# Kernel tuning notes

Measured on AMD Instinct MI355X. Metric: run time of the kernel, lower is better.

## Reference

```python
import math
import jax, jax.numpy as jnp
import numpy as np

ANCHOR_AREAS = [4 * 4, 16 * 16, 64 * 64, 128 * 128]
ASPECT_RATIOS = [1 / 2.0, 1 / 1.0, 2 / 1.0]
SCALE_RATIOS = [1.0, 2.0, 3 / 4.0]
NUM_ANCHORS = len(ASPECT_RATIOS) * len(SCALE_RATIOS)  # 9


def _anchor_wh():
    wh = []
    for s in ANCHOR_AREAS:
        for ar in ASPECT_RATIOS:
            h = math.sqrt(s / ar)
            w = ar * h
            for sr in SCALE_RATIOS:
                wh.append([w * sr, h * sr])
    return np.asarray(wh, np.float32).reshape(len(ANCHOR_AREAS), NUM_ANCHORS, 2)


def build_anchor_boxes(input_size):
    """All anchors in (cx, cy, w, h), shape [A, 4]. Static numpy computation."""
    wh = _anchor_wh()
    out = []
    for i in range(len(ANCHOR_AREAS)):
        fm = int(math.ceil(input_size / 2.0 ** (i + 2)))
        grid = input_size / fm
        centers = (np.arange(fm, dtype=np.float32) + 0.5) * grid
        gx, gy = np.meshgrid(centers, centers)  # gx varies along width
        xy = np.stack([gx, gy], axis=-1)  # [fm, fm, 2]
        xy = np.broadcast_to(xy[:, :, None, :], (fm, fm, NUM_ANCHORS, 2))
        whl = np.broadcast_to(wh[i][None, None, :, :], (fm, fm, NUM_ANCHORS, 2))
        out.append(np.concatenate([xy, whl], axis=-1).reshape(-1, 4))
    return jnp.asarray(np.concatenate(out, 0), jnp.float32)


def box_iou_xywh(anchors, boxes):
    """anchors [A,4] xywh, boxes [B,N,4] xywh -> IoU [B,A,N] (kuangliu +1 convention)."""
    a1 = jnp.concatenate([anchors[:, :2] - anchors[:, 2:] / 2,
                          anchors[:, :2] + anchors[:, 2:] / 2], axis=-1)  # [A,4]
    b1 = jnp.concatenate([boxes[..., :2] - boxes[..., 2:] / 2,
                          boxes[..., :2] + boxes[..., 2:] / 2], axis=-1)  # [B,N,4]
    lt = jnp.maximum(a1[None, :, None, :2], b1[:, None, :, :2])  # [B,A,N,2]
    rb = jnp.minimum(a1[None, :, None, 2:], b1[:, None, :, 2:])
    wh = jnp.clip(rb - lt + 1.0, 0.0)
    inter = wh[..., 0] * wh[..., 1]  # [B,A,N]
    area_a = (a1[:, 2] - a1[:, 0] + 1.0) * (a1[:, 3] - a1[:, 1] + 1.0)  # [A]
    area_b = (b1[..., 2] - b1[..., 0] + 1.0) * (b1[..., 3] - b1[..., 1] + 1.0)  # [B,N]
    return inter / (area_a[None, :, None] + area_b[:, None, :] - inter)


def setup_inputs() -> dict:
    key = jax.random.key(0)
    k1, k2, k3 = jax.random.split(key, 3)
    B, N, S = 4, 64, 512
    # valid xyxy boxes inside the image
    x1y1 = jax.random.uniform(k1, (B, N, 2), jnp.float32, 0.0, S - 130.0)
    wh = jax.random.uniform(k2, (B, N, 2), jnp.float32, 4.0, 128.0)
    boxes = jnp.concatenate([x1y1, x1y1 + wh], axis=-1)
    labels = jax.random.randint(k3, (B, N), 0, 10, jnp.int64 if jax.config.jax_enable_x64 else jnp.int32)
    return {"labels": labels, "boxes": boxes, "input_size": S}


def reference(labels, boxes, input_size):
    B = boxes.shape[0]
    anchors = build_anchor_boxes(int(input_size))  # [A,4] xywh
    # xyxy -> xywh (kuangliu: center (a+b)/2, size b-a+1)
    a, b = boxes[..., :2], boxes[..., 2:]
    boxes_xywh = jnp.concatenate([(a + b) / 2.0, b - a + 1.0], axis=-1)  # [B,N,4]
    ious = box_iou_xywh(anchors, boxes_xywh)  # [B,A,N]
    max_ious = jnp.max(ious, axis=2)  # [B,A]
    max_ids = jnp.argmax(ious, axis=2)  # [B,A]
    gather = jax.vmap(lambda t, i: t[i])
    matched = gather(boxes_xywh, max_ids)  # [B,A,4]
    loc_xy = (matched[..., :2] - anchors[None, :, :2]) / anchors[None, :, 2:]
    loc_wh = jnp.log(matched[..., 2:] / anchors[None, :, 2:])
    loc_targets = jnp.concatenate([loc_xy, loc_wh], axis=-1)  # [B,A,4]
    cls = gather(labels, max_ids)  # [B,A]
    cls = jnp.where(max_ious < 0.5, 0, cls)
    cls = jnp.where((max_ious > 0.4) & (max_ious < 0.5), -1, cls)
    return cls, loc_targets
```

## Files before the change

### kernel.cpp

```cpp
#include <hip/hip_runtime.h>
#include <math.h>


__global__ __launch_bounds__(256) void anchors_kernel(
    const int*   __restrict__ labels,
    const float* __restrict__ boxes,
    float*       __restrict__ out,
    int B, int N, int A, int S)
{
    __shared__ float4 s_corn[256];
    __shared__ float  s_area[256];
    __shared__ float4 s_xywh[256];
    __shared__ int    s_lab[256];
    __shared__ float4 s_b0[4];
    __shared__ int    s_l0[4];

    const int t    = threadIdx.x;
    const int lane = t & 63;
    const int wid  = t >> 6;
    const int gid  = blockIdx.x * 256 + t;

    const int b  = (blockIdx.x * 256) / A;
    int r0 = blockIdx.x * 256 - b * A;
    int lvl = 0, fm = S >> 2;
    #pragma unroll
    for (int i = 0; i < 3; ++i) {
        int cnt = fm * fm * 9;
        if (r0 >= cnt) { r0 -= cnt; lvl = i + 1; fm >>= 1; }
    }
    const int   lfm  = 31 - __clz(fm);
    const float grid = (float)(4 << lvl);
    const float sl   = (float)((lvl == 3) ? 128 : (4 << (2 * lvl)));

    const int wr0     = r0 + wid * 64;
    const int cell_lo = wr0 / 9;
    const int cell_hi = (wr0 + 63) / 9;
    const int ci_lo = cell_lo >> lfm, ci_hi = cell_hi >> lfm;
    int cj_lo, cj_hi;
    if (ci_lo == ci_hi) { cj_lo = cell_lo & (fm - 1); cj_hi = cell_hi & (fm - 1); }
    else                { cj_lo = 0;                  cj_hi = fm - 1; }
    const float ext  = 1.41422f * sl + 0.5f;
    const float bbx1 = ((float)cj_lo + 0.5f) * grid - ext;
    const float bbx2 = ((float)cj_hi + 0.5f) * grid + ext;
    const float bby1 = ((float)ci_lo + 0.5f) * grid - ext;
    const float bby2 = ((float)ci_hi + 0.5f) * grid + ext;

    int L;
    {
        bool  pred = false;
        float cx = 0, cy = 0, w = 0, h = 0, bx1 = 0, by1 = 0, bx2 = 0, by2 = 0;
        int   lab = 0;
        if (lane < N) {
            float4 bx = reinterpret_cast<const float4*>(boxes)[b * N + lane];
            cx = (bx.x + bx.z) * 0.5f;
            cy = (bx.y + bx.w) * 0.5f;
            w  = bx.z - bx.x + 1.0f;
            h  = bx.w - bx.y + 1.0f;
            bx1 = cx - w * 0.5f;  by1 = cy - h * 0.5f;
            bx2 = cx + w * 0.5f;  by2 = cy + h * 0.5f;
            lab = labels[b * N + lane];
            pred = (fminf(bbx2, bx2) - fmaxf(bbx1, bx1) + 1.0f > 0.0f) &&
                   (fminf(bby2, by2) - fmaxf(bby1, by1) + 1.0f > 0.0f);
        }
        unsigned long long mask = __ballot(pred);
        if (pred) {
            int pos = wid * 64 + __popcll(mask & ((1ull << lane) - 1ull));
            s_corn[pos] = make_float4(bx1, by1, bx2, by2);
            s_area[pos] = (bx2 - bx1 + 1.0f) * (by2 - by1 + 1.0f);
            s_xywh[pos] = make_float4(cx, cy, w, h);
            s_lab[pos]  = lab;
        }
        if (lane == 0) { s_b0[wid] = make_float4(cx, cy, w, h); s_l0[wid] = lab; }
        L = __popcll(mask);
    }

    const int r    = r0 + t;
    const int k    = r % 9;
    const int cell = r / 9;
    const int cj   = cell & (fm - 1);
    const int ci   = cell >> lfm;

    const int ar_i = (k >= 6) ? 2 : ((k >= 3) ? 1 : 0);
    const int sr_i = k - 3 * ar_i;
    const double s2  = sqrt(2.0);
    const double hb  = (ar_i == 0) ? s2 : (ar_i == 1 ? 1.0 : 0.5 * s2);
    const double wb  = (ar_i == 0) ? 0.5 * s2 : (ar_i == 1 ? 1.0 : s2);
    const double srd = (sr_i == 0) ? 1.0 : (sr_i == 1 ? 2.0 : 0.75);
    const float  aw  = (float)(wb * srd) * sl;
    const float  ah  = (float)(hb * srd) * sl;

    const float acx = ((float)cj + 0.5f) * grid;
    const float acy = ((float)ci + 0.5f) * grid;
    const float ax1 = acx - aw * 0.5f;
    const float ay1 = acy - ah * 0.5f;
    const float ax2 = acx + aw * 0.5f;
    const float ay2 = acy + ah * 0.5f;
    const float area_a = (ax2 - ax1 + 1.0f) * (ay2 - ay1 + 1.0f);

    float best_in = 0.0f, best_un = 1.0f;
    int   bj = -1;
    const int base = wid * 64;
    for (int j = 0; j < L; ++j) {
        float4 c = s_corn[base + j];
        float iw = fmaxf(fminf(ax2, c.z) - fmaxf(ax1, c.x) + 1.0f, 0.0f);
        float ih = fmaxf(fminf(ay2, c.w) - fmaxf(ay1, c.y) + 1.0f, 0.0f);
        float in_ = iw * ih;
        float un_ = (area_a + s_area[base + j]) - in_;
        bool better = (in_ * best_un) > (best_in * un_);
        best_in = better ? in_ : best_in;
        best_un = better ? un_ : best_un;
        bj      = better ? j   : bj;
    }

    float best, mcx, mcy, mw, mh;
    int lab;
    if (bj >= 0) {
        best = best_in / best_un;
        float4 m = s_xywh[base + bj];
        mcx = m.x; mcy = m.y; mw = m.z; mh = m.w;
        lab = s_lab[base + bj];
    } else {
        best = 0.0f;
        float4 m = s_b0[wid];
        mcx = m.x; mcy = m.y; mw = m.z; mh = m.w;
        lab = s_l0[wid];
    }

    int cls = lab;
    if (best < 0.5f) cls = 0;
    if (best > 0.4f && best < 0.5f) cls = -1;

    const float rcp_aw = __builtin_amdgcn_rcpf(aw);
    const float rcp_ah = __builtin_amdgcn_rcpf(ah);
    float4 loc;
    loc.x = (mcx - acx) * rcp_aw;
    loc.y = (mcy - acy) * rcp_ah;
    loc.z = __logf(mw * rcp_aw);
    loc.w = __logf(mh * rcp_ah);

    if (gid < B * A) {
        out[(size_t)gid] = (float)cls;
        reinterpret_cast<float4*>(out + (size_t)B * A)[gid] = loc;
    }
}

extern "C" void kernel_launch(void* const* d_in, const int* in_sizes, int n_in,
                              void* d_out, int out_size, void* d_ws, size_t ws_size,
                              hipStream_t stream) {
    const int S = 512;
    int A = 0;
    for (int i = 0; i < 4; ++i) {
        int f = (S + (1 << (i + 2)) - 1) >> (i + 2);
        A += f * f * 9;
    }
    const int B = out_size / (5 * A);
    const int N = in_sizes[0] / B;

    const int total  = B * A;
    const int blocks = (total + 255) / 256;

    anchors_kernel<<<blocks, 256, 0, stream>>>(
        (const int*)d_in[0], (const float*)d_in[1], (float*)d_out, B, N, A, S);
}
```

Before: 17.34 us.

## Coarsen threads to four anchors each with per-wave 256-anchor chunks and 2D grid

Each wave now handles a contiguous chunk of 256 anchors, four per lane, and the batch index comes from blockIdx.y instead of a division. The box load, culling ballot and shared-memory compaction are done once per 256 anchors rather than once per 64, and the inner IoU loop reuses each loaded candidate box across four anchors for more instruction-level parallelism. In exchange, the culling bounding box covers a wider span of anchors, so each wave may keep more candidate boxes, and about a quarter as many threads are launched.

```diff
diff --git a/kernel.cpp b/kernel.cpp
--- a/kernel.cpp
+++ b/kernel.cpp
@@ -18,10 +18,12 @@
     const int t    = threadIdx.x;
     const int lane = t & 63;
     const int wid  = t >> 6;
-    const int gid  = blockIdx.x * 256 + t;
+    const int b    = blockIdx.y;
 
-    const int b  = (blockIdx.x * 256) / A;
-    int r0 = blockIdx.x * 256 - b * A;
+    const int wr0 = (blockIdx.x * 4 + wid) * 256;
+    if (wr0 >= A) return;
+
+    int r0 = wr0;
     int lvl = 0, fm = S >> 2;
     #pragma unroll
     for (int i = 0; i < 3; ++i) {
@@ -32,9 +34,8 @@
     const float grid = (float)(4 << lvl);
     const float sl   = (float)((lvl == 3) ? 128 : (4 << (2 * lvl)));
 
-    const int wr0     = r0 + wid * 64;
-    const int cell_lo = wr0 / 9;
-    const int cell_hi = (wr0 + 63) / 9;
+    const int cell_lo = r0 / 9;
+    const int cell_hi = (r0 + 255) / 9;
     const int ci_lo = cell_lo >> lfm, ci_hi = cell_hi >> lfm;
     int cj_lo, cj_hi;
     if (ci_lo == ci_hi) { cj_lo = cell_lo & (fm - 1); cj_hi = cell_hi & (fm - 1); }
@@ -74,73 +75,81 @@
         L = __popcll(mask);
     }
 
-    const int r    = r0 + t;
-    const int k    = r % 9;
-    const int cell = r / 9;
-    const int cj   = cell & (fm - 1);
-    const int ci   = cell >> lfm;
+    float ax1[4], ay1[4], ax2[4], ay2[4], areaA[4];
+    float awv[4], ahv[4], acxv[4], acyv[4];
+    #pragma unroll
+    for (int q = 0; q < 4; ++q) {
+        const int r    = r0 + 64 * q + lane;
+        const int cell = r / 9;
+        const int kk   = r - cell * 9;
+        const int cj   = cell & (fm - 1);
+        const int ci   = cell >> lfm;
+        const int ar_i = (kk >= 6) ? 2 : ((kk >= 3) ? 1 : 0);
+        const int sr_i = kk - 3 * ar_i;
+        const double s2  = 1.4142135623730951;
+        const double hb  = (ar_i == 0) ? s2 : (ar_i == 1 ? 1.0 : 0.5 * s2);
+        const double wb  = (ar_i == 0) ? 0.5 * s2 : (ar_i == 1 ? 1.0 : s2);
+        const double srd = (sr_i == 0) ? 1.0 : (sr_i == 1 ? 2.0 : 0.75);
+        const float aw  = (float)(wb * srd) * sl;
+        const float ah  = (float)(hb * srd) * sl;
+        const float acx = ((float)cj + 0.5f) * grid;
+        const float acy = ((float)ci + 0.5f) * grid;
+        awv[q] = aw; ahv[q] = ah; acxv[q] = acx; acyv[q] = acy;
+        ax1[q] = acx - aw * 0.5f;  ay1[q] = acy - ah * 0.5f;
+        ax2[q] = acx + aw * 0.5f;  ay2[q] = acy + ah * 0.5f;
+        areaA[q] = (ax2[q] - ax1[q] + 1.0f) * (ay2[q] - ay1[q] + 1.0f);
+    }
 
-    const int ar_i = (k >= 6) ? 2 : ((k >= 3) ? 1 : 0);
-    const int sr_i = k - 3 * ar_i;
-    const double s2  = sqrt(2.0);
-    const double hb  = (ar_i == 0) ? s2 : (ar_i == 1 ? 1.0 : 0.5 * s2);
-    const double wb  = (ar_i == 0) ? 0.5 * s2 : (ar_i == 1 ? 1.0 : s2);
-    const double srd = (sr_i == 0) ? 1.0 : (sr_i == 1 ? 2.0 : 0.75);
-    const float  aw  = (float)(wb * srd) * sl;
-    const float  ah  = (float)(hb * srd) * sl;
-
-    const float acx = ((float)cj + 0.5f) * grid;
-    const float acy = ((float)ci + 0.5f) * grid;
-    const float ax1 = acx - aw * 0.5f;
-    const float ay1 = acy - ah * 0.5f;
-    const float ax2 = acx + aw * 0.5f;
-    const float ay2 = acy + ah * 0.5f;
-    const float area_a = (ax2 - ax1 + 1.0f) * (ay2 - ay1 + 1.0f);
-
-    float best_in = 0.0f, best_un = 1.0f;
-    int   bj = -1;
+    float bin[4] = {0.0f, 0.0f, 0.0f, 0.0f};
+    float bun[4] = {1.0f, 1.0f, 1.0f, 1.0f};
+    int   bj[4]  = {-1, -1, -1, -1};
     const int base = wid * 64;
     for (int j = 0; j < L; ++j) {
-        float4 c = s_corn[base + j];
-        float iw = fmaxf(fminf(ax2, c.z) - fmaxf(ax1, c.x) + 1.0f, 0.0f);
-        float ih = fmaxf(fminf(ay2, c.w) - fmaxf(ay1, c.y) + 1.0f, 0.0f);
-        float in_ = iw * ih;
-        float un_ = (area_a + s_area[base + j]) - in_;
-        bool better = (in_ * best_un) > (best_in * un_);
-        best_in = better ? in_ : best_in;
-        best_un = better ? un_ : best_un;
-        bj      = better ? j   : bj;
+        float4 c  = s_corn[base + j];
+        float  ab = s_area[base + j];
+        #pragma unroll
+        for (int q = 0; q < 4; ++q) {
+            float iw = fmaxf(fminf(ax2[q], c.z) - fmaxf(ax1[q], c.x) + 1.0f, 0.0f);
+            float ih = fmaxf(fminf(ay2[q], c.w) - fmaxf(ay1[q], c.y) + 1.0f, 0.0f);
+            float in_ = iw * ih;
+            float un_ = (areaA[q] + ab) - in_;
+            bool better = (in_ * bun[q]) > (bin[q] * un_);
+            bin[q] = better ? in_ : bin[q];
+            bun[q] = better ? un_ : bun[q];
+            bj[q]  = better ? j   : bj[q];
+        }
     }
 
-    float best, mcx, mcy, mw, mh;
-    int lab;
-    if (bj >= 0) {
-        best = best_in / best_un;
-        float4 m = s_xywh[base + bj];
-        mcx = m.x; mcy = m.y; mw = m.z; mh = m.w;
-        lab = s_lab[base + bj];
-    } else {
-        best = 0.0f;
-        float4 m = s_b0[wid];
-        mcx = m.x; mcy = m.y; mw = m.z; mh = m.w;
-        lab = s_l0[wid];
-    }
+    #pragma unroll
+    for (int q = 0; q < 4; ++q) {
+        float best, mcx, mcy, mw, mh;
+        int lab;
+        if (bj[q] >= 0) {
+            best = bin[q] / bun[q];
+            float4 m = s_xywh[base + bj[q]];
+            mcx = m.x; mcy = m.y; mw = m.z; mh = m.w;
+            lab = s_lab[base + bj[q]];
+        } else {
+            best = 0.0f;
+            float4 m = s_b0[wid];
+            mcx = m.x; mcy = m.y; mw = m.z; mh = m.w;
+            lab = s_l0[wid];
+        }
+        int cls = lab;
+        if (best < 0.5f) cls = 0;
+        if (best > 0.4f && best < 0.5f) cls = -1;
 
-    int cls = lab;
-    if (best < 0.5f) cls = 0;
-    if (best > 0.4f && best < 0.5f) cls = -1;
+        const float rcp_aw = __builtin_amdgcn_rcpf(awv[q]);
+        const float rcp_ah = __builtin_amdgcn_rcpf(ahv[q]);
+        float4 loc;
+        loc.x = (mcx - acxv[q]) * rcp_aw;
+        loc.y = (mcy - acyv[q]) * rcp_ah;
+        loc.z = __logf(mw * rcp_aw);
+        loc.w = __logf(mh * rcp_ah);
 
-    const float rcp_aw = __builtin_amdgcn_rcpf(aw);
-    const float rcp_ah = __builtin_amdgcn_rcpf(ah);
-    float4 loc;
-    loc.x = (mcx - acx) * rcp_aw;
-    loc.y = (mcy - acy) * rcp_ah;
-    loc.z = __logf(mw * rcp_aw);
-    loc.w = __logf(mh * rcp_ah);
-
-    if (gid < B * A) {
-        out[(size_t)gid] = (float)cls;
-        reinterpret_cast<float4*>(out + (size_t)B * A)[gid] = loc;
+        const size_t gidq = (size_t)b * A + (size_t)(wr0 + 64 * q + lane);
+        out[gidq] = (float)cls;
+        reinterpret_cast<float4*>(out + (size_t)B * A)[gidq] = loc;
     }
 }
 
@@ -156,9 +165,10 @@
     const int B = out_size / (5 * A);
     const int N = in_sizes[0] / B;
 
-    const int total  = B * A;
-    const int blocks = (total + 255) / 256;
+    const int chunks  = A / 256;
+    const int blocksX = (chunks + 3) / 4;
+    dim3 gridDim(blocksX, B);
 
-    anchors_kernel<<<blocks, 256, 0, stream>>>(
+    anchors_kernel<<<gridDim, 256, 0, stream>>>(
         (const int*)d_in[0], (const float*)d_in[1], (float*)d_out, B, N, A, S);
 }
```

After: 22.60 us. +30.3%, slower.

## Use 2D grid with 1024-thread blocks and constant anchor-size tables

Applied to the files above, without the earlier changes.

Switches the launch to a 2D grid (anchor chunks by batch) with 1024-thread blocks, so each wave derives its own level and batch and exits early past A. The double-precision sqrt/multiply used for anchor sizes is replaced with float constant selects. The per-wave box culling test now runs on the raw xyxy box before the xywh conversion, with a wider margin. Larger blocks reduce the block count but may lower occupancy flexibility.

```diff
diff --git a/kernel.cpp b/kernel.cpp
--- a/kernel.cpp
+++ b/kernel.cpp
@@ -2,26 +2,28 @@
 #include <math.h>
 
 
-__global__ __launch_bounds__(256) void anchors_kernel(
+__global__ __launch_bounds__(1024) void anchors_kernel(
     const int*   __restrict__ labels,
     const float* __restrict__ boxes,
     float*       __restrict__ out,
     int B, int N, int A, int S)
 {
-    __shared__ float4 s_corn[256];
-    __shared__ float  s_area[256];
-    __shared__ float4 s_xywh[256];
-    __shared__ int    s_lab[256];
-    __shared__ float4 s_b0[4];
-    __shared__ int    s_l0[4];
+    __shared__ float4 s_corn[1024];
+    __shared__ float  s_area[1024];
+    __shared__ float4 s_xywh[1024];
+    __shared__ int    s_lab[1024];
+    __shared__ float4 s_b0[16];
+    __shared__ int    s_l0[16];
 
     const int t    = threadIdx.x;
     const int lane = t & 63;
     const int wid  = t >> 6;
-    const int gid  = blockIdx.x * 256 + t;
+    const int b    = blockIdx.y;
 
-    const int b  = (blockIdx.x * 256) / A;
-    int r0 = blockIdx.x * 256 - b * A;
+    const int wr0 = blockIdx.x * 1024 + wid * 64;
+    if (wr0 >= A) return;
+
+    int r0 = wr0;
     int lvl = 0, fm = S >> 2;
     #pragma unroll
     for (int i = 0; i < 3; ++i) {
@@ -32,14 +34,13 @@
     const float grid = (float)(4 << lvl);
     const float sl   = (float)((lvl == 3) ? 128 : (4 << (2 * lvl)));
 
-    const int wr0     = r0 + wid * 64;
-    const int cell_lo = wr0 / 9;
-    const int cell_hi = (wr0 + 63) / 9;
+    const int cell_lo = r0 / 9;
+    const int cell_hi = (r0 + 63) / 9;
     const int ci_lo = cell_lo >> lfm, ci_hi = cell_hi >> lfm;
     int cj_lo, cj_hi;
     if (ci_lo == ci_hi) { cj_lo = cell_lo & (fm - 1); cj_hi = cell_hi & (fm - 1); }
     else                { cj_lo = 0;                  cj_hi = fm - 1; }
-    const float ext  = 1.41422f * sl + 0.5f;
+    const float ext  = 1.41422f * sl + 2.0f;
     const float bbx1 = ((float)cj_lo + 0.5f) * grid - ext;
     const float bbx2 = ((float)cj_hi + 0.5f) * grid + ext;
     const float bby1 = ((float)ci_lo + 0.5f) * grid - ext;
@@ -52,6 +53,8 @@
         int   lab = 0;
         if (lane < N) {
             float4 bx = reinterpret_cast<const float4*>(boxes)[b * N + lane];
+            pred = (fminf(bbx2, bx.z) - fmaxf(bbx1, bx.x) + 1.0f > 0.0f) &&
+                   (fminf(bby2, bx.w) - fmaxf(bby1, bx.y) + 1.0f > 0.0f);
             cx = (bx.x + bx.z) * 0.5f;
             cy = (bx.y + bx.w) * 0.5f;
             w  = bx.z - bx.x + 1.0f;
@@ -59,8 +62,6 @@
             bx1 = cx - w * 0.5f;  by1 = cy - h * 0.5f;
             bx2 = cx + w * 0.5f;  by2 = cy + h * 0.5f;
             lab = labels[b * N + lane];
-            pred = (fminf(bbx2, bx2) - fmaxf(bbx1, bx1) + 1.0f > 0.0f) &&
-                   (fminf(bby2, by2) - fmaxf(bby1, by1) + 1.0f > 0.0f);
         }
         unsigned long long mask = __ballot(pred);
         if (pred) {
@@ -74,20 +75,30 @@
         L = __popcll(mask);
     }
 
-    const int r    = r0 + t;
-    const int k    = r % 9;
+    const int r    = r0 + lane;
     const int cell = r / 9;
+    const int k    = r - cell * 9;
     const int cj   = cell & (fm - 1);
     const int ci   = cell >> lfm;
 
-    const int ar_i = (k >= 6) ? 2 : ((k >= 3) ? 1 : 0);
-    const int sr_i = k - 3 * ar_i;
-    const double s2  = sqrt(2.0);
-    const double hb  = (ar_i == 0) ? s2 : (ar_i == 1 ? 1.0 : 0.5 * s2);
-    const double wb  = (ar_i == 0) ? 0.5 * s2 : (ar_i == 1 ? 1.0 : s2);
-    const double srd = (sr_i == 0) ? 1.0 : (sr_i == 1 ? 2.0 : 0.75);
-    const float  aw  = (float)(wb * srd) * sl;
-    const float  ah  = (float)(hb * srd) * sl;
+    const float cwk =
+        (k < 3) ? ((k == 0) ? 0.70710678118654752f
+                 : (k == 1) ? 1.41421356237309515f
+                            : 0.53033008588991064f)
+      : (k < 6) ? ((k == 3) ? 1.0f : (k == 4) ? 2.0f : 0.75f)
+                : ((k == 6) ? 1.41421356237309515f
+                 : (k == 7) ? 2.82842712474619029f
+                            : 1.06066017177982129f);
+    const float chk =
+        (k < 3) ? ((k == 0) ? 1.41421356237309515f
+                 : (k == 1) ? 2.82842712474619029f
+                            : 1.06066017177982129f)
+      : (k < 6) ? ((k == 3) ? 1.0f : (k == 4) ? 2.0f : 0.75f)
+                : ((k == 6) ? 0.70710678118654752f
+                 : (k == 7) ? 1.41421356237309515f
+                            : 0.53033008588991064f);
+    const float aw = cwk * sl;
+    const float ah = chk * sl;
 
     const float acx = ((float)cj + 0.5f) * grid;
     const float acy = ((float)ci + 0.5f) * grid;
@@ -138,10 +149,9 @@
     loc.z = __logf(mw * rcp_aw);
     loc.w = __logf(mh * rcp_ah);
 
-    if (gid < B * A) {
-        out[(size_t)gid] = (float)cls;
-        reinterpret_cast<float4*>(out + (size_t)B * A)[gid] = loc;
-    }
+    const size_t gid = (size_t)b * A + (size_t)(wr0 + lane);
+    out[gid] = (float)cls;
+    reinterpret_cast<float4*>(out + (size_t)B * A)[gid] = loc;
 }
 
 extern "C" void kernel_launch(void* const* d_in, const int* in_sizes, int n_in,
@@ -156,9 +166,8 @@
     const int B = out_size / (5 * A);
     const int N = in_sizes[0] / B;
 
-    const int total  = B * A;
-    const int blocks = (total + 255) / 256;
+    dim3 gridDim((A + 1023) / 1024, B);
 
-    anchors_kernel<<<blocks, 256, 0, stream>>>(
+    anchors_kernel<<<gridDim, 1024, 0, stream>>>(
         (const int*)d_in[0], (const float*)d_in[1], (float*)d_out, B, N, A, S);
 }
```

After: 23.97 us. 38.2% more time.
